# Performance work log

Measured on AMD Instinct MI355X. Metric: run time of the kernel, lower is better.

The kernel has to match this reference:

```python
import jax, jax.numpy as jnp
import numpy as np

L, H, O, S, B = 128, 1024, 64, 256, 512  # latent, hidden, output, seq_len, batch
IN0 = L + O  # LSTM layer-0 input size


def setup_inputs() -> dict:
    key = jax.random.key(0)
    ks = jax.random.split(key, 16)
    sc = 0.05
    n = lambda k, shape: (jax.random.normal(k, shape, jnp.float32) * sc)
    return {
        "z": jax.random.normal(ks[0], (B, L), jnp.float32),
        "Wh": n(ks[1], (H, L)), "bh": jnp.zeros((H,), jnp.float32),
        "Wc": n(ks[2], (H, L)), "bc": jnp.zeros((H,), jnp.float32),
        "Wih0": n(ks[3], (4 * H, IN0)), "Whh0": n(ks[4], (4 * H, H)),
        "bih0": n(ks[5], (4 * H,)), "bhh0": n(ks[6], (4 * H,)),
        "Wih1": n(ks[7], (4 * H, H)), "Whh1": n(ks[8], (4 * H, H)),
        "bih1": n(ks[9], (4 * H,)), "bhh1": n(ks[10], (4 * H,)),
        "Wout": n(ks[11], (O, H)), "bout": jnp.zeros((O,), jnp.float32),
    }


def _lstm_cell(x, h, c, Wih, Whh, b):
    # PyTorch gate order: i, f, g, o
    gates = x @ Wih.T + h @ Whh.T + b  # (B, 4H)
    i, f, g, o = jnp.split(gates, 4, axis=-1)
    c_new = jax.nn.sigmoid(f) * c + jax.nn.sigmoid(i) * jnp.tanh(g)
    h_new = jax.nn.sigmoid(o) * jnp.tanh(c_new)
    return h_new, c_new


def reference(z, Wh, bh, Wc, bc, Wih0, Whh0, bih0, bhh0, Wih1, Whh1, bih1, bhh1, Wout, bout):
    batch = z.shape[0]
    # h_0 / c_0 are the same projection repeated for both layers
    h0 = z @ Wh.T + bh  # (B, H)
    c0 = z @ Wc.T + bc
    b0 = bih0 + bhh0
    b1 = bih1 + bhh1

    def step(carry, _):
        h1, c1, h2, c2, inp = carry
        x = jnp.concatenate([z, inp], axis=-1)  # (B, L+O)
        h1n, c1n = _lstm_cell(x, h1, c1, Wih0, Whh0, b0)
        h2n, c2n = _lstm_cell(h1n, h2, c2, Wih1, Whh1, b1)
        out = h2n @ Wout.T + bout  # (B, O) feeds back as next input
        return (h1n, c1n, h2n, c2n, out), out

    init = (h0, c0, h0, c0, jnp.zeros((batch, Wout.shape[0]), z.dtype))
    _, outs = jax.lax.scan(step, init, None, length=S)  # (S, B, O)
    return jnp.transpose(outs, (1, 0, 2))  # (B, S, O)
```

## Files before the change

### kernel.cpp

```cpp
#include <hip/hip_runtime.h>

#define Lz   128
#define Hd   1024
#define Od   64
#define Sq   256
#define Bt   512
#define K1   1216
#define K2q  2048
#define G4H  4096
#define NBLK 256u

typedef __attribute__((ext_vector_type(8))) short  short8;
typedef __attribute__((ext_vector_type(4))) float  floatx4;

__device__ __forceinline__ short f2bf(float x) {
  unsigned u = __float_as_uint(x);
  unsigned r = (u + 0x7fffu + ((u >> 16) & 1u)) >> 16;
  return (short)r;
}
__device__ __forceinline__ float sigf(float x)   { return 1.0f / (1.0f + __expf(-x)); }
__device__ __forceinline__ float tanhf_(float x) { return 1.0f - 2.0f / (__expf(2.0f * x) + 1.0f); }

__device__ __forceinline__ void gl_lds_z(const short* g, void* l) {
  __builtin_amdgcn_global_load_lds(
      (__attribute__((address_space(1))) const void*)g,
      (__attribute__((address_space(3))) void*)l, 16, 0, 0);
}
__device__ __forceinline__ void gl_lds_a(const short* g, void* l) {
  __builtin_amdgcn_global_load_lds(
      (__attribute__((address_space(1))) const void*)g,
      (__attribute__((address_space(3))) void*)l, 16, 0, 1);
}
__device__ __forceinline__ void gl_lds_w(const short* g, void* l) {
  __builtin_amdgcn_global_load_lds(
      (__attribute__((address_space(1))) const void*)g,
      (__attribute__((address_space(3))) void*)l, 16, 0, 16);
}
__device__ __forceinline__ void st_wt(short* p, short v) {
  asm volatile("global_store_short %0, %1, off sc0"
               :: "v"(p), "v"((unsigned)(unsigned short)v) : "memory");
}

#define S_BARRIER() asm volatile("s_barrier" ::: "memory")
#define WAITVM(n)   asm volatile("s_waitcnt vmcnt(" #n ")" ::: "memory")

__device__ __forceinline__ void xbar(int* b) {
  __syncthreads();
  if (threadIdx.x == 0) {
    unsigned* cnt = (unsigned*)b;
    unsigned* gen = (unsigned*)b + 1;
    unsigned g = __hip_atomic_load(gen, __ATOMIC_RELAXED, __HIP_MEMORY_SCOPE_AGENT);
    unsigned a = __hip_atomic_fetch_add(cnt, 1u, __ATOMIC_RELAXED, __HIP_MEMORY_SCOPE_AGENT);
    if (a == 31u) {
      __hip_atomic_store(cnt, 0u, __ATOMIC_RELAXED, __HIP_MEMORY_SCOPE_AGENT);
      __hip_atomic_store(gen, g + 1u, __ATOMIC_RELAXED, __HIP_MEMORY_SCOPE_AGENT);
    } else {
      while (__hip_atomic_load(gen, __ATOMIC_RELAXED, __HIP_MEMORY_SCOPE_AGENT) == g)
        __builtin_amdgcn_s_sleep(8);
    }
  }
  __syncthreads();
}

__device__ __forceinline__ int oldrow(int nr) {
  int bn = nr >> 6, rem = nr & 63, g = rem >> 4, jj = rem & 15;
  return g * Hd + bn * 16 + jj;
}

struct Params {
  const short *W1r, *W2r, *Woutb;
  const float *b0v, *b1v, *bout;
  short *A1_0, *A1_1, *A2_0, *A2_1;
  float *c1, *c2, *out;
  int *barr;
};

__global__ void k_conv_w1a(const float* __restrict__ Whh0, short* __restrict__ W1r) {
  int idx = blockIdx.x * 256 + threadIdx.x;
  int nr = idx >> 10, k = idx & 1023;
  W1r[nr * K1 + k] = f2bf(Whh0[oldrow(nr) * Hd + k]);
}
__global__ void k_conv_w1c(const float* __restrict__ Wih0, short* __restrict__ W1r) {
  int idx = blockIdx.x * 256 + threadIdx.x;
  int nr = idx >> 7, kz = idx & 127;
  W1r[nr * K1 + 1024 + kz] = f2bf(Wih0[oldrow(nr) * (Lz + Od) + kz]);
}
__global__ void k_conv_w1d(const float* __restrict__ Wih0, short* __restrict__ W1r) {
  int idx = blockIdx.x * 256 + threadIdx.x;
  int nr = idx >> 6, j = idx & 63;
  W1r[nr * K1 + 1152 + j] = f2bf(Wih0[oldrow(nr) * (Lz + Od) + Lz + j]);
}
__global__ void k_conv_w2(const float* __restrict__ Wih1, const float* __restrict__ Whh1,
                          short* __restrict__ W2r) {
  int idx = blockIdx.x * 256 + threadIdx.x;
  int nr = idx >> 11, k = idx & 2047;
  int orow = oldrow(nr);
  float v = (k < Hd) ? Wih1[orow * Hd + k] : Whh1[orow * Hd + (k - Hd)];
  W2r[nr * K2q + k] = f2bf(v);
}
__global__ void k_conv_wout(const float* __restrict__ Wout, short* __restrict__ Woutb) {
  int idx = blockIdx.x * 256 + threadIdx.x;
  Woutb[idx] = f2bf(Wout[idx]);
}
__global__ void k_vec(const float* __restrict__ bih0, const float* __restrict__ bhh0,
                      const float* __restrict__ bih1, const float* __restrict__ bhh1,
                      float* __restrict__ b0v, float* __restrict__ b1v,
                      int* __restrict__ barzero) {
  int n = blockIdx.x * 256 + threadIdx.x;
  if (n < 256) barzero[n] = 0;
  b0v[n] = bih0[n] + bhh0[n];
  b1v[n] = bih1[n] + bhh1[n];
}
__global__ void k_init(const float* __restrict__ z, const float* __restrict__ Wh,
                       const float* __restrict__ bh, const float* __restrict__ Wc,
                       const float* __restrict__ bc,
                       short* __restrict__ A1_0, short* __restrict__ A2_0,
                       float* __restrict__ c1, float* __restrict__ c2) {
  int idx = blockIdx.x * 256 + threadIdx.x;
  int m = idx >> 10, n = idx & 1023;
  const float* zr = z + m * Lz;
  const float* whr = Wh + n * Lz;
  const float* wcr = Wc + n * Lz;
  float hh = bh[n], cc = bc[n];
  #pragma unroll 8
  for (int k = 0; k < Lz; ++k) { float zv = zr[k]; hh += zv * whr[k]; cc += zv * wcr[k]; }
  c1[idx] = cc;
  c2[idx] = cc;
  short hb = f2bf(hh);
  A1_0[m * K1 + n] = hb;
  if (n < Od) A1_0[m * K1 + 1152 + n] = 0;
  A2_0[m * K2q + Hd + n] = hb;
}
__global__ void k_initz(const float* __restrict__ z, short* __restrict__ A1_0,
                        short* __restrict__ A1_1) {
  int idx = blockIdx.x * 256 + threadIdx.x;
  int m = idx >> 7, k = idx & 127;
  short v = f2bf(z[idx]);
  A1_0[m * K1 + 1024 + k] = v;
  A1_1[m * K1 + 1024 + k] = v;
}

#define MFMA16(a, b, c) __builtin_amdgcn_mfma_f32_16x16x32_bf16(a, b, c, 0, 0, 0)
#define BUFSH 12288
#define NBUF  5
#define LDS_BYTES (NBUF * BUFSH * 2)

__device__ __forceinline__ void out_reg(const short* __restrict__ h2src,
    const short* __restrict__ Wo, const float* __restrict__ boutv,
    float* __restrict__ outp, int tt, int mo,
    short* __restrict__ ofb, int tid, int* __restrict__ ocnt)
{
  const int lane = tid & 63, w = tid >> 6;
  const int l15 = lane & 15, q = lane >> 4;
  const short* ap = h2src + (size_t)(mo + l15) * K2q + Hd + q * 8;
  const short* bp = Wo + (size_t)(w * 16 + l15) * Hd + q * 8;
  floatx4 acc = {};
  short8 A0, B0, A1, B1, A2, B2, A3, B3;
#define OLA(r, kk) asm volatile("global_load_dwordx4 %0, %1, off sc0" \
    : "=v"(r) : "v"(ap + (kk) * 32) : "memory")
#define OLB(r, kk) asm volatile("global_load_dwordx4 %0, %1, off" \
    : "=v"(r) : "v"(bp + (kk) * 32) : "memory")
  OLA(A0, 0); OLB(B0, 0); OLA(A1, 1); OLB(B1, 1);
  OLA(A2, 2); OLB(B2, 2); OLA(A3, 3); OLB(B3, 3);
  #pragma unroll
  for (int g = 0; g < 16; g += 2) {
    WAITVM(4); __builtin_amdgcn_sched_barrier(0);
    acc = MFMA16(A0, B0, acc); acc = MFMA16(A1, B1, acc);
    if (g + 2 < 16) { OLA(A0, 2*(g+2)); OLB(B0, 2*(g+2));
                      OLA(A1, 2*(g+2)+1); OLB(B1, 2*(g+2)+1); }
    if (g + 3 < 16) { WAITVM(4); } else { WAITVM(0); }
    __builtin_amdgcn_sched_barrier(0);
    acc = MFMA16(A2, B2, acc); acc = MFMA16(A3, B3, acc);
    if (g + 3 < 16) { OLA(A2, 2*(g+3)); OLB(B2, 2*(g+3));
                      OLA(A3, 2*(g+3)+1); OLB(B3, 2*(g+3)+1); }
  }
#undef OLA
#undef OLB
  #pragma unroll
  for (int r = 0; r < 4; ++r) {
    int m = mo + q * 4 + r;
    int n = w * 16 + l15;
    float v = acc[r] + boutv[n];
    outp[(size_t)m * (Sq * Od) + (size_t)tt * Od + n] = v;
    if (ofb) st_wt(ofb + (size_t)m * K1 + 1152 + n, f2bf(v));
  }
  WAITVM(0);
  __syncthreads();
  if (ocnt && tid == 0)
    __hip_atomic_fetch_add(ocnt, 1, __ATOMIC_RELAXED, __HIP_MEMORY_SCOPE_AGENT);
}

__device__ __forceinline__ void gemm_win(
    const short* __restrict__ Asrc, int astride, int nk, int zstart,
    const short* __restrict__ Wsrc,
    const float* __restrict__ bz, float cr[2][4],
    short* __restrict__ hd0, int hs0, int ho0,
    short* __restrict__ hd1, int hs1, int ho1,
    int m0, int bn2, short* sm, int tid,
    int* __restrict__ ocnt, int othresh)
{
  const int lane = tid & 63, w = tid >> 6;
  const int l15 = lane & 15, q = lane >> 4;
  const int mh = w >> 1, gh = w & 1;
  floatx4 acc[2][4] = {};

  const short* Ab = Asrc + (size_t)m0 * astride;
  const short* Wb = Wsrc + (size_t)(bn2 * 128) * astride;

  auto stage = [&](int kk, int b) {
    const int kb = kk * 64;
    short* as = sm + b * BUFSH;
    short* ws = as + 4096;
    const bool stat = (kk == zstart) || (kk == zstart + 1);
    #pragma unroll
    for (int i = 0; i < 2; ++i) {
      int s = i * 256 + tid;
      int row = s >> 3, cg = (s & 7) ^ (row & 7);
      const short* gp = Ab + (size_t)row * astride + kb + cg * 8;
      if (stat) gl_lds_z(gp, as + s * 8);
      else      gl_lds_a(gp, as + s * 8);
    }
    #pragma unroll
    for (int i = 0; i < 4; ++i) {
      int s = i * 256 + tid;
      int row = s >> 3, cg = (s & 7) ^ (row & 7);
      gl_lds_w(Wb + (size_t)row * astride + kb + cg * 8, ws + s * 8);
    }
  };

  stage(0, 0);
  stage(1, 1);
  stage(2, 2);
  for (int kk = 0; kk < nk; ++kk) {
    if (kk + 3 < nk) {
      if (ocnt && kk + 3 == nk - 1) {
        while (__hip_atomic_load(ocnt, __ATOMIC_RELAXED, __HIP_MEMORY_SCOPE_AGENT) < othresh)
          __builtin_amdgcn_s_sleep(1);
      }
      stage(kk + 3, (kk + 3) % NBUF);
      WAITVM(18);
    }
    else if (kk + 2 < nk) { WAITVM(12); }
    else if (kk + 1 < nk) { WAITVM(6); }
    else { WAITVM(0); }
    S_BARRIER();
    const short* as = sm + (kk % NBUF) * BUFSH;
    const short* ws = as + 4096;
    #pragma unroll
    for (int ks = 0; ks < 2; ++ks) {
      const int cc = ks * 4 + q;
      short8 a[2];
      #pragma unroll
      for (int mt = 0; mt < 2; ++mt) {
        const int ra = mh * 32 + mt * 16 + l15;
        a[mt] = *(const short8*)(as + (ra * 8 + (cc ^ (ra & 7))) * 8);
      }
      #pragma unroll
      for (int g = 0; g < 4; ++g) {
        const int rw = gh * 64 + g * 16 + l15;
        short8 b = *(const short8*)(ws + (rw * 8 + (cc ^ (rw & 7))) * 8);
        acc[0][g] = MFMA16(a[0], b, acc[0][g]);
        acc[1][g] = MFMA16(a[1], b, acc[1][g]);
      }
    }
  }
  #pragma unroll
  for (int mt = 0; mt < 2; ++mt) {
    #pragma unroll
    for (int r = 0; r < 4; ++r) {
      const int mg = m0 + mh * 32 + mt * 16 + q * 4 + r;
      const int colh = bn2 * 32 + gh * 16 + l15;
      float iv = acc[mt][0][r] + bz[0];
      float fv = acc[mt][1][r] + bz[1];
      float gv = acc[mt][2][r] + bz[2];
      float ov = acc[mt][3][r] + bz[3];
      float cn = sigf(fv) * cr[mt][r] + sigf(iv) * tanhf_(gv);
      cr[mt][r] = cn;
      short hb = f2bf(sigf(ov) * tanhf_(cn));
      st_wt(hd0 + (size_t)mg * hs0 + ho0 + colh, hb);
      if (hd1) st_wt(hd1 + (size_t)mg * hs1 + ho1 + colh, hb);
    }
  }
}

__global__ __launch_bounds__(256, 1) void lstm_main(Params p) {
  extern __shared__ __align__(16) short smem[];
  const int tid = threadIdx.x;

  __shared__ int sh_ids[2];
  if (tid == 0) {
    unsigned xr;
    asm volatile("s_getreg_b32 %0, hwreg(HW_REG_XCC_ID)" : "=s"(xr));
    int xcc = (int)(xr & 7u);
    int slot = (int)__hip_atomic_fetch_add((unsigned*)(p.barr + xcc * 16 + 3), 1u,
                                           __ATOMIC_RELAXED, __HIP_MEMORY_SCOPE_AGENT);
    sh_ids[0] = xcc;
    sh_ids[1] = slot & 31;
  }
  __syncthreads();
  const int xcc  = sh_ids[0];
  const int slot = sh_ids[1];
  int* xb = p.barr + xcc * 16;

  const int m0 = xcc * 64;
  const int bn2 = slot;
  const bool ojob = ((slot & 7) == 0);
  const int mo = xcc * 64 + (slot >> 3) * 16;

  const int lane = tid & 63, w = tid >> 6;
  const int l15 = lane & 15, q = lane >> 4;
  const int mh = w >> 1, gh = w & 1;
  const int colh = bn2 * 32 + gh * 16 + l15;

  float bA[4], bB[4], c1r[2][4], c2r[2][4];
  #pragma unroll
  for (int g = 0; g < 4; ++g) {
    bA[g] = p.b0v[g * Hd + colh];
    bB[g] = p.b1v[g * Hd + colh];
  }
  #pragma unroll
  for (int mt = 0; mt < 2; ++mt)
    #pragma unroll
    for (int r = 0; r < 4; ++r) {
      const int mg = m0 + mh * 32 + mt * 16 + q * 4 + r;
      c1r[mt][r] = p.c1[mg * Hd + colh];
      c2r[mt][r] = p.c2[mg * Hd + colh];
    }

  for (int t = 0; t < Sq; ++t) {
    const int par = t & 1;
    const short* A1p = par ? p.A1_1 : p.A1_0;
    short* A1n = par ? p.A1_0 : p.A1_1;
    short* A2p = par ? p.A2_1 : p.A2_0;
    short* A2n = par ? p.A2_0 : p.A2_1;
    if (ojob && t > 0)
      out_reg(A2p, p.Woutb, p.bout, p.out, t - 1, mo, (short*)A1p, tid, xb + 2);
    gemm_win(A1p, K1, 19, 16, p.W1r, bA, c1r,
             A1n, K1, 0, (short*)A2p, K2q, 0, m0, bn2, smem, tid,
             xb + 2, 4 * t);
    xbar(xb);
    gemm_win(A2p, K2q, 32, -2, p.W2r, bB, c2r,
             A2n, K2q, Hd, (short*)nullptr, 0, 0, m0, bn2, smem, tid,
             nullptr, 0);
    xbar(xb);
  }
  if (ojob)
    out_reg(p.A2_0, p.Woutb, p.bout, p.out, Sq - 1, mo, (short*)nullptr, tid, nullptr);
}

extern "C" void kernel_launch(void* const* d_in, const int* in_sizes, int n_in,
                              void* d_out, int out_size, void* d_ws, size_t ws_size,
                              hipStream_t stream) {
  const float* z    = (const float*)d_in[0];
  const float* Wh   = (const float*)d_in[1];
  const float* bh   = (const float*)d_in[2];
  const float* Wc   = (const float*)d_in[3];
  const float* bc   = (const float*)d_in[4];
  const float* Wih0 = (const float*)d_in[5];
  const float* Whh0 = (const float*)d_in[6];
  const float* bih0 = (const float*)d_in[7];
  const float* bhh0 = (const float*)d_in[8];
  const float* Wih1 = (const float*)d_in[9];
  const float* Whh1 = (const float*)d_in[10];
  const float* bih1 = (const float*)d_in[11];
  const float* bhh1 = (const float*)d_in[12];
  const float* Wout = (const float*)d_in[13];
  const float* bout = (const float*)d_in[14];
  float* out = (float*)d_out;

  char* ws = (char*)d_ws;
  size_t off = 0;
  auto carve = [&](size_t bytes) { char* p = ws + off; off = (off + bytes + 255) & ~size_t(255); return p; };
  short* W1r   = (short*)carve((size_t)G4H * K1 * 2);
  short* W2r   = (short*)carve((size_t)G4H * K2q * 2);
  short* Woutb = (short*)carve((size_t)Od * Hd * 2);
  float* b0v   = (float*)carve(G4H * 4);
  float* b1v   = (float*)carve(G4H * 4);
  short* A1_0  = (short*)carve((size_t)Bt * K1 * 2);
  short* A1_1  = (short*)carve((size_t)Bt * K1 * 2);
  short* A2_0  = (short*)carve((size_t)Bt * K2q * 2);
  short* A2_1  = (short*)carve((size_t)Bt * K2q * 2);
  float* c1    = (float*)carve((size_t)Bt * Hd * 4);
  float* c2    = (float*)carve((size_t)Bt * Hd * 4);
  int*   barr  = (int*)carve(1024);

  k_conv_w1a<<<16384, 256, 0, stream>>>(Whh0, W1r);
  k_conv_w1c<<<2048, 256, 0, stream>>>(Wih0, W1r);
  k_conv_w1d<<<1024, 256, 0, stream>>>(Wih0, W1r);
  k_conv_w2 <<<32768, 256, 0, stream>>>(Wih1, Whh1, W2r);
  k_conv_wout<<<256, 256, 0, stream>>>(Wout, Woutb);
  k_vec<<<16, 256, 0, stream>>>(bih0, bhh0, bih1, bhh1, b0v, b1v, barr);
  k_init<<<2048, 256, 0, stream>>>(z, Wh, bh, Wc, bc, A1_0, A2_0, c1, c2);
  k_initz<<<256, 256, 0, stream>>>(z, A1_0, A1_1);

  Params pr{W1r, W2r, Woutb, b0v, b1v, bout,
            A1_0, A1_1, A2_0, A2_1, c1, c2, out, barr};

  (void)hipFuncSetAttribute((const void*)lstm_main,
                            hipFuncAttributeMaxDynamicSharedMemorySize, LDS_BYTES);
  lstm_main<<<dim3(NBLK), dim3(256), LDS_BYTES, stream>>>(pr);
}
```

Measured before the change: 11.07 ms.

## Load activation fragments directly to registers and deepen weight LDS pipeline

The activation (A) operand no longer goes through LDS. Each lane now loads its MFMA fragments straight from global memory into registers, double-buffered across k-chunks. Only weight tiles are staged in LDS, now with 8 buffers and a 4-chunk prefetch depth, and the per-chunk vmcnt waits are recomputed for the new load counts. This is meant to remove LDS traffic and LDS reads for A and to hide weight-load latency better, at the cost of more VGPRs and uncoalesced, latency-exposed global loads for the activations.

```diff
diff --git a/kernel.cpp b/kernel.cpp
--- a/kernel.cpp
+++ b/kernel.cpp
@@ -21,16 +21,6 @@
 __device__ __forceinline__ float sigf(float x)   { return 1.0f / (1.0f + __expf(-x)); }
 __device__ __forceinline__ float tanhf_(float x) { return 1.0f - 2.0f / (__expf(2.0f * x) + 1.0f); }
 
-__device__ __forceinline__ void gl_lds_z(const short* g, void* l) {
-  __builtin_amdgcn_global_load_lds(
-      (__attribute__((address_space(1))) const void*)g,
-      (__attribute__((address_space(3))) void*)l, 16, 0, 0);
-}
-__device__ __forceinline__ void gl_lds_a(const short* g, void* l) {
-  __builtin_amdgcn_global_load_lds(
-      (__attribute__((address_space(1))) const void*)g,
-      (__attribute__((address_space(3))) void*)l, 16, 0, 1);
-}
 __device__ __forceinline__ void gl_lds_w(const short* g, void* l) {
   __builtin_amdgcn_global_load_lds(
       (__attribute__((address_space(1))) const void*)g,
@@ -141,9 +131,17 @@
 }
 
 #define MFMA16(a, b, c) __builtin_amdgcn_mfma_f32_16x16x32_bf16(a, b, c, 0, 0, 0)
-#define BUFSH 12288
-#define NBUF  5
-#define LDS_BYTES (NBUF * BUFSH * 2)
+#define WBUF  8192
+#define NBUF  8
+#define LDS_BYTES (NBUF * WBUF * 2)
+
+#define LDA4(d0, d1, d2, d3, p00, p01, p10, p11, ck) do {                       \
+  const int _o = (ck) * 64;                                                     \
+  asm volatile("global_load_dwordx4 %0, %1, off sc0" : "=v"(d0) : "v"((p00)+_o) : "memory"); \
+  asm volatile("global_load_dwordx4 %0, %1, off sc0" : "=v"(d1) : "v"((p01)+_o) : "memory"); \
+  asm volatile("global_load_dwordx4 %0, %1, off sc0" : "=v"(d2) : "v"((p10)+_o) : "memory"); \
+  asm volatile("global_load_dwordx4 %0, %1, off sc0" : "=v"(d3) : "v"((p11)+_o) : "memory"); \
+} while (0)
 
 __device__ __forceinline__ void out_reg(const short* __restrict__ h2src,
     const short* __restrict__ Wo, const float* __restrict__ boutv,
@@ -191,7 +189,7 @@
 }
 
 __device__ __forceinline__ void gemm_win(
-    const short* __restrict__ Asrc, int astride, int nk, int zstart,
+    const short* __restrict__ Asrc, int astride, int nk,
     const short* __restrict__ Wsrc,
     const float* __restrict__ bz, float cr[2][4],
     short* __restrict__ hd0, int hs0, int ho0,
@@ -207,63 +205,79 @@
   const short* Ab = Asrc + (size_t)m0 * astride;
   const short* Wb = Wsrc + (size_t)(bn2 * 128) * astride;
 
-  auto stage = [&](int kk, int b) {
-    const int kb = kk * 64;
-    short* as = sm + b * BUFSH;
-    short* ws = as + 4096;
-    const bool stat = (kk == zstart) || (kk == zstart + 1);
-    #pragma unroll
-    for (int i = 0; i < 2; ++i) {
-      int s = i * 256 + tid;
-      int row = s >> 3, cg = (s & 7) ^ (row & 7);
-      const short* gp = Ab + (size_t)row * astride + kb + cg * 8;
-      if (stat) gl_lds_z(gp, as + s * 8);
-      else      gl_lds_a(gp, as + s * 8);
-    }
+  const short* a00 = Ab + (size_t)(mh * 32 + l15) * astride + q * 8;
+  const short* a01 = a00 + 32;
+  const short* a10 = a00 + (size_t)16 * astride;
+  const short* a11 = a10 + 32;
+
+  auto stageW = [&](int ck, int b) {
+    short* ws = sm + b * WBUF;
     #pragma unroll
     for (int i = 0; i < 4; ++i) {
       int s = i * 256 + tid;
       int row = s >> 3, cg = (s & 7) ^ (row & 7);
-      gl_lds_w(Wb + (size_t)row * astride + kb + cg * 8, ws + s * 8);
+      gl_lds_w(Wb + (size_t)row * astride + ck * 64 + cg * 8, ws + s * 8);
     }
   };
-
-  stage(0, 0);
-  stage(1, 1);
-  stage(2, 2);
-  for (int kk = 0; kk < nk; ++kk) {
-    if (kk + 3 < nk) {
-      if (ocnt && kk + 3 == nk - 1) {
-        while (__hip_atomic_load(ocnt, __ATOMIC_RELAXED, __HIP_MEMORY_SCOPE_AGENT) < othresh)
-          __builtin_amdgcn_s_sleep(1);
-      }
-      stage(kk + 3, (kk + 3) % NBUF);
-      WAITVM(18);
-    }
-    else if (kk + 2 < nk) { WAITVM(12); }
-    else if (kk + 1 < nk) { WAITVM(6); }
-    else { WAITVM(0); }
-    S_BARRIER();
-    const short* as = sm + (kk % NBUF) * BUFSH;
-    const short* ws = as + 4096;
+  auto guard = [&](int ck) {
+    if (ocnt && ck == nk - 1) {
+      while (__hip_atomic_load(ocnt, __ATOMIC_RELAXED, __HIP_MEMORY_SCOPE_AGENT) < othresh)
+        __builtin_amdgcn_s_sleep(1);
+    }
+  };
+  auto computeC = [&](const short8& f00, const short8& f01,
+                      const short8& f10, const short8& f11, const short* ws) {
     #pragma unroll
     for (int ks = 0; ks < 2; ++ks) {
       const int cc = ks * 4 + q;
-      short8 a[2];
-      #pragma unroll
-      for (int mt = 0; mt < 2; ++mt) {
-        const int ra = mh * 32 + mt * 16 + l15;
-        a[mt] = *(const short8*)(as + (ra * 8 + (cc ^ (ra & 7))) * 8);
-      }
+      const short8 a0 = ks ? f01 : f00;
+      const short8 a1 = ks ? f11 : f10;
       #pragma unroll
       for (int g = 0; g < 4; ++g) {
         const int rw = gh * 64 + g * 16 + l15;
         short8 b = *(const short8*)(ws + (rw * 8 + (cc ^ (rw & 7))) * 8);
-        acc[0][g] = MFMA16(a[0], b, acc[0][g]);
-        acc[1][g] = MFMA16(a[1], b, acc[1][g]);
+        acc[0][g] = MFMA16(a0, b, acc[0][g]);
+        acc[1][g] = MFMA16(a1, b, acc[1][g]);
       }
     }
-  }
+  };
+
+  short8 x00, x01, x10, x11, y00, y01, y10, y11;
+
+  LDA4(x00, x01, x10, x11, a00, a01, a10, a11, 0);
+  stageW(0, 0); stageW(1, 1); stageW(2, 2); stageW(3, 3);
+
+  for (int kk = 0; kk < nk; kk += 2) {
+    {
+      const int cL = kk + 1;
+      if (cL < nk) { guard(cL); LDA4(y00, y01, y10, y11, a00, a01, a10, a11, cL); }
+      const int cW = kk + 4;
+      if (cW < nk) stageW(cW, cW & 7);
+      if (kk == 0)            { WAITVM(20); }
+      else if (kk + 4 < nk)   { WAITVM(12); }
+      else if (kk + 3 < nk)   { WAITVM(8);  }
+      else if (kk + 1 < nk)   { WAITVM(4);  }
+      else                    { WAITVM(0);  }
+      __builtin_amdgcn_sched_barrier(0);
+      S_BARRIER();
+      computeC(x00, x01, x10, x11, sm + (kk & 7) * WBUF);
+    }
+    const int k1 = kk + 1;
+    if (k1 < nk) {
+      const int cL = k1 + 1;
+      if (cL < nk) { guard(cL); LDA4(x00, x01, x10, x11, a00, a01, a10, a11, cL); }
+      const int cW = k1 + 4;
+      if (cW < nk) stageW(cW, cW & 7);
+      if (k1 + 4 < nk)        { WAITVM(12); }
+      else if (k1 + 3 < nk)   { WAITVM(8);  }
+      else if (k1 + 1 < nk)   { WAITVM(4);  }
+      else                    { WAITVM(0);  }
+      __builtin_amdgcn_sched_barrier(0);
+      S_BARRIER();
+      computeC(y00, y01, y10, y11, sm + (k1 & 7) * WBUF);
+    }
+  }
+
   #pragma unroll
   for (int mt = 0; mt < 2; ++mt) {
     #pragma unroll
@@ -335,11 +349,11 @@
     short* A2n = par ? p.A2_0 : p.A2_1;
     if (ojob && t > 0)
       out_reg(A2p, p.Woutb, p.bout, p.out, t - 1, mo, (short*)A1p, tid, xb + 2);
-    gemm_win(A1p, K1, 19, 16, p.W1r, bA, c1r,
+    gemm_win(A1p, K1, 19, p.W1r, bA, c1r,
              A1n, K1, 0, (short*)A2p, K2q, 0, m0, bn2, smem, tid,
              xb + 2, 4 * t);
     xbar(xb);
-    gemm_win(A2p, K2q, 32, -2, p.W2r, bB, c2r,
+    gemm_win(A2p, K2q, 32, p.W2r, bB, c2r,
              A2n, K2q, Hd, (short*)nullptr, 0, 0, m0, bn2, smem, tid,
              nullptr, 0);
     xbar(xb);
```

After: 13.12 ms. 1.19x slower.
